# Performance work log

Hardware: AMD Instinct MI355X
Metric: run time of the kernel (lower is better)

Reference implementation:

```python
import jax, jax.numpy as jnp
import numpy as np

B, F, D = 1024, 64, 64  # batch, num fields, embedding dim


def setup_inputs() -> dict:
    key = jax.random.key(0)
    ks = jax.random.split(key, 7)
    return {
        "x": jax.random.normal(ks[0], (B, F, D), dtype=jnp.float32),
        "W1": jax.random.normal(ks[1], (F, F * F), dtype=jnp.float32) * 0.02,
        "b1": jax.random.normal(ks[2], (F,), dtype=jnp.float32) * 0.02,
        "W2": jax.random.normal(ks[3], (F, F * F), dtype=jnp.float32) * 0.02,
        "b2": jax.random.normal(ks[4], (F,), dtype=jnp.float32) * 0.02,
        "Wfc": jax.random.normal(ks[5], (1, 2 * F), dtype=jnp.float32) * 0.02,
        "bfc": jax.random.normal(ks[6], (1,), dtype=jnp.float32) * 0.02,
    }


def reference(x, W1, b1, W2, b2, Wfc, bfc):
    # x: [B, F, D]. CIN layer: outer product over field dims, 1x1 conv (channel
    # contraction with weight [F, F*F]), ReLU.
    b_, f0, d = x.shape
    x0 = x[:, :, None, :]  # [B, F, 1, D]
    h = x
    xs = []
    for W, b in ((W1, b1), (W2, b2)):
        z = (x0 * h[:, None, :, :]).reshape(b_, f0 * f0, d)  # [B, F*F, D]
        h = jax.nn.relu(jnp.einsum('oc,bcd->bod', W, z) + b[None, :, None])  # [B, F, D]
        xs.append(h)
    pooled = jnp.sum(jnp.concatenate(xs, axis=1), axis=2)  # [B, 2F] sum-pool over D
    return pooled @ Wfc.T + bfc  # [B, 1]
```

## Files before the change

### kernel.cpp

```cpp
#include <hip/hip_runtime.h>

typedef short s16x4 __attribute__((ext_vector_type(4)));
typedef short s16x8 __attribute__((ext_vector_type(8)));
typedef float f32x2 __attribute__((ext_vector_type(2)));
typedef float f32x16 __attribute__((ext_vector_type(16)));
typedef unsigned int u32x4 __attribute__((ext_vector_type(4)));

#define HT_STRIDE 72

__device__ __forceinline__ unsigned short f2bf(float f) {
    unsigned int u = __float_as_uint(f);
    u += 0x7fffu + ((u >> 16) & 1u);
    return (unsigned short)(u >> 16);
}
__device__ __forceinline__ float bf2f(unsigned short h) {
    return __uint_as_float(((unsigned int)h) << 16);
}
__device__ __forceinline__ unsigned int pk2bf_rne(float lo, float hi) {
    unsigned int a = __float_as_uint(lo);
    a += 0x7fffu + ((a >> 16) & 1u);
    unsigned int b = __float_as_uint(hi);
    b += 0x7fffu + ((b >> 16) & 1u);
    return (a >> 16) | (b & 0xffff0000u);
}

__global__ __launch_bounds__(256) void prepack_kernel(const float* __restrict__ W1,
                                                      const float* __restrict__ W2,
                                                      unsigned short* __restrict__ Wp) {
    int tid = blockIdx.x * 256 + threadIdx.x;
    int lane = tid & 63;
    int ks = (tid >> 6) & 3;
    int jt = (tid >> 8) & 1;
    int o = (tid >> 9) & 63;
    int l = tid >> 15;
    int q2 = lane >> 5;
    int n31 = lane & 31;
    const float* W = l ? W2 : W1;
    const float* base = W + o * 4096 + jt * 32 + n31;
    int i0 = 16 * ks + 8 * q2;
    float v[8];
#pragma unroll
    for (int t = 0; t < 8; ++t) v[t] = base[(i0 + t) * 64];
    u32x4 pv;
    pv[0] = pk2bf_rne(v[0], v[1]);
    pv[1] = pk2bf_rne(v[2], v[3]);
    pv[2] = pk2bf_rne(v[4], v[5]);
    pv[3] = pk2bf_rne(v[6], v[7]);
    ((u32x4*)Wp)[tid] = pv;
}

__global__ __launch_bounds__(256, 2) void cin_kernel(const float* __restrict__ x,
                                                     const unsigned short* __restrict__ Wp,
                                                     const float* __restrict__ b1,
                                                     const float* __restrict__ b2,
                                                     const float* __restrict__ Wfc,
                                                     const float* __restrict__ bfc,
                                                     float* __restrict__ out) {
    __shared__ __align__(16) unsigned short sH[2][2][64 * HT_STRIDE];
    __shared__ float sBias[128], sWfc[128], sRed[4];

    const int tid = threadIdx.x;
    const int w = tid >> 6;
    const int lane = tid & 63;
    const int q2 = lane >> 5;
    const int n31 = lane & 31;
    const int b_loc = w & 1;
    const int oh = w >> 1;
    const int bb = blockIdx.x;

#pragma unroll
    for (int bl = 0; bl < 2; ++bl) {
        const float4* xb4 = (const float4*)(x + (bb * 2 + bl) * 4096);
#pragma unroll
        for (int rr = 0; rr < 4; ++rr) {
            int e4 = rr * 256 + tid;
            float4 v = xb4[e4];
            int e = e4 << 2;
            int f = e >> 6;
            int d0 = e & 63;
            sH[0][bl][(d0 + 0) * HT_STRIDE + f] = f2bf(v.x);
            sH[0][bl][(d0 + 1) * HT_STRIDE + f] = f2bf(v.y);
            sH[0][bl][(d0 + 2) * HT_STRIDE + f] = f2bf(v.z);
            sH[0][bl][(d0 + 3) * HT_STRIDE + f] = f2bf(v.w);
        }
    }
    if (tid < 128) {
        sBias[tid] = (tid < 64) ? b1[tid] : b2[tid - 64];
        sWfc[tid] = Wfc[tid];
    }
    __syncthreads();

    const f32x16 zz = {};
    float contrib = 0.0f;
    const s16x8* WpS8 = (const s16x8*)Wp;

    s16x8 bfr[2][4];
#pragma unroll
    for (int nt = 0; nt < 2; ++nt) {
        const int d = nt * 32 + n31;
#pragma unroll
        for (int ks = 0; ks < 4; ++ks)
            bfr[nt][ks] = *(const s16x8*)&sH[0][b_loc][d * HT_STRIDE + 16 * ks + 8 * q2];
    }

    for (int l = 0; l < 2; ++l) {
        if (l) __syncthreads();

        const unsigned short* hsrc = sH[l][b_loc];
        f32x2 cw[2][2][8];
#pragma unroll
        for (int nt = 0; nt < 2; ++nt) {
            const int d = nt * 32 + n31;
#pragma unroll
            for (int jt = 0; jt < 2; ++jt)
#pragma unroll
                for (int m = 0; m < 4; ++m) {
                    s16x4 hv = *(const s16x4*)&hsrc[d * HT_STRIDE + jt * 32 + 4 * q2 + 8 * m];
                    cw[nt][jt][2 * m] = (f32x2){bf2f((unsigned short)hv[0]),
                                                bf2f((unsigned short)hv[1])};
                    cw[nt][jt][2 * m + 1] = (f32x2){bf2f((unsigned short)hv[2]),
                                                    bf2f((unsigned short)hv[3])};
                }
        }

        s16x8 Areg[2][4];
        {
            const int F0 = (l * 128 + 2 * oh) * 4;
            const s16x8* p = WpS8 + F0 * 64 + lane;
#pragma unroll
            for (int ks = 0; ks < 4; ++ks) Areg[0][ks] = p[ks * 64];
        }
        f32x2 hp[2];

#pragma unroll 2
        for (int it = 0; it < 64; ++it) {
            const int oc = it >> 1, jt = it & 1;
            const int o = 2 * oc + oh;
            if (it < 63) {
                const int itn = it + 1;
                const int on = 2 * (itn >> 1) + oh;
                const int Fn = (l * 128 + 2 * on + (itn & 1)) * 4;
                const s16x8* p = WpS8 + Fn * 64 + lane;
#pragma unroll
                for (int ks = 0; ks < 4; ++ks) Areg[(it + 1) & 1][ks] = p[ks * 64];
            }
            const s16x8* A = Areg[it & 1];

            f32x16 a0 = __builtin_amdgcn_mfma_f32_32x32x16_bf16(A[0], bfr[0][0], zz, 0, 0, 0);
            f32x16 a1 = __builtin_amdgcn_mfma_f32_32x32x16_bf16(A[0], bfr[1][0], zz, 0, 0, 0);
#pragma unroll
            for (int ks = 1; ks < 4; ++ks) {
                a0 = __builtin_amdgcn_mfma_f32_32x32x16_bf16(A[ks], bfr[0][ks], a0, 0, 0, 0);
                a1 = __builtin_amdgcn_mfma_f32_32x32x16_bf16(A[ks], bfr[1][ks], a1, 0, 0, 0);
            }

#pragma unroll
            for (int nt = 0; nt < 2; ++nt) {
                const f32x2* a2 = nt ? (const f32x2*)&a1 : (const f32x2*)&a0;
                f32x2 s = a2[0] * cw[nt][jt][0];
#pragma unroll
                for (int p = 1; p < 8; ++p) s += a2[p] * cw[nt][jt][p];
                if (jt == 0) {
                    hp[nt] = s;
                } else {
                    f32x2 t2 = hp[nt] + s;
                    float hsum = t2.x + t2.y;
                    hsum += __shfl_xor(hsum, 32, 64);
                    float v = fmaxf(hsum + sBias[l * 64 + o], 0.0f);
                    contrib += v * sWfc[l * 64 + o];
                    if (l == 0)
                        sH[1][b_loc][(nt * 32 + n31) * HT_STRIDE + o] = f2bf(v);
                }
            }
        }
    }

    contrib *= 0.5f;
#pragma unroll
    for (int off = 32; off > 0; off >>= 1)
        contrib += __shfl_down(contrib, off, 64);
    if (lane == 0) sRed[w] = contrib;
    __syncthreads();
    if (tid < 2)
        out[bb * 2 + tid] = sRed[tid] + sRed[tid + 2] + bfc[0];
}

extern "C" void kernel_launch(void* const* d_in, const int* in_sizes, int n_in,
                              void* d_out, int out_size, void* d_ws, size_t ws_size,
                              hipStream_t stream) {
    const float* x = (const float*)d_in[0];
    const float* W1 = (const float*)d_in[1];
    const float* b1 = (const float*)d_in[2];
    const float* W2 = (const float*)d_in[3];
    const float* b2 = (const float*)d_in[4];
    const float* Wfc = (const float*)d_in[5];
    const float* bfc = (const float*)d_in[6];
    float* out = (float*)d_out;

    unsigned short* Wp = (unsigned short*)d_ws;

    prepack_kernel<<<256, 256, 0, stream>>>(W1, W2, Wp);
    cin_kernel<<<512, 256, 0, stream>>>(x, Wp, b1, b2, Wfc, bfc, out);
}
```

Baseline: 137.8 us.

## Split CIN work one batch per block with four waves over output channels

Each block now handles a single batch element, with its four waves splitting the 64 output channels into groups of four instead of two batches times two channel halves. The grid doubles to 1024 blocks, LDS per block halves, and launch bounds allow four blocks per CU, so more work is in flight and each wave runs half as many MFMA iterations. The prepack kernel now stages a full weight row in LDS for coalesced reads and writes the bf16 fragments in a layout ordered by wave group, so each wave streams its weights contiguously. The trade-off is that each weight fragment is now loaded once per batch element rather than being shared across two batches in a block, which doubles weight traffic through L2.

```diff
diff --git a/kernel.cpp b/kernel.cpp
--- a/kernel.cpp
+++ b/kernel.cpp
@@ -27,50 +27,55 @@
 __global__ __launch_bounds__(256) void prepack_kernel(const float* __restrict__ W1,
                                                       const float* __restrict__ W2,
                                                       unsigned short* __restrict__ Wp) {
-    int tid = blockIdx.x * 256 + threadIdx.x;
-    int lane = tid & 63;
-    int ks = (tid >> 6) & 3;
-    int jt = (tid >> 8) & 1;
-    int o = (tid >> 9) & 63;
-    int l = tid >> 15;
-    int q2 = lane >> 5;
-    int n31 = lane & 31;
+    __shared__ float sRow[4096];
+    const int blk = blockIdx.x;
+    const int l = blk >> 6, o = blk & 63;
     const float* W = l ? W2 : W1;
-    const float* base = W + o * 4096 + jt * 32 + n31;
-    int i0 = 16 * ks + 8 * q2;
-    float v[8];
-#pragma unroll
-    for (int t = 0; t < 8; ++t) v[t] = base[(i0 + t) * 64];
-    u32x4 pv;
-    pv[0] = pk2bf_rne(v[0], v[1]);
-    pv[1] = pk2bf_rne(v[2], v[3]);
-    pv[2] = pk2bf_rne(v[4], v[5]);
-    pv[3] = pk2bf_rne(v[6], v[7]);
-    ((u32x4*)Wp)[tid] = pv;
-}
-
-__global__ __launch_bounds__(256, 2) void cin_kernel(const float* __restrict__ x,
+    const float4* src = (const float4*)(W + o * 4096);
+    float4* dstL = (float4*)sRow;
+#pragma unroll
+    for (int r = 0; r < 4; ++r)
+        dstL[r * 256 + threadIdx.x] = src[r * 256 + threadIdx.x];
+    __syncthreads();
+    const int oh = o & 3, oc = o >> 2;
+#pragma unroll
+    for (int s = 0; s < 2; ++s) {
+        int sl = s * 256 + threadIdx.x;
+        int lane = sl & 63;
+        int ks = (sl >> 6) & 3;
+        int jt = sl >> 8;
+        int q2 = lane >> 5, n31 = lane & 31;
+        const float* base = sRow + jt * 32 + n31;
+        int i0 = 16 * ks + 8 * q2;
+        u32x4 pv;
+        pv[0] = pk2bf_rne(base[(i0 + 0) * 64], base[(i0 + 1) * 64]);
+        pv[1] = pk2bf_rne(base[(i0 + 2) * 64], base[(i0 + 3) * 64]);
+        pv[2] = pk2bf_rne(base[(i0 + 4) * 64], base[(i0 + 5) * 64]);
+        pv[3] = pk2bf_rne(base[(i0 + 6) * 64], base[(i0 + 7) * 64]);
+        int G = (((l * 4 + oh) * 16 + oc) * 2 + jt) * 4 + ks;
+        ((u32x4*)Wp)[G * 64 + lane] = pv;
+    }
+}
+
+__global__ __launch_bounds__(256, 4) void cin_kernel(const float* __restrict__ x,
                                                      const unsigned short* __restrict__ Wp,
                                                      const float* __restrict__ b1,
                                                      const float* __restrict__ b2,
                                                      const float* __restrict__ Wfc,
                                                      const float* __restrict__ bfc,
                                                      float* __restrict__ out) {
-    __shared__ __align__(16) unsigned short sH[2][2][64 * HT_STRIDE];
+    __shared__ __align__(16) unsigned short sH[2][64 * HT_STRIDE];
     __shared__ float sBias[128], sWfc[128], sRed[4];
 
     const int tid = threadIdx.x;
-    const int w = tid >> 6;
+    const int oh = tid >> 6;
     const int lane = tid & 63;
     const int q2 = lane >> 5;
     const int n31 = lane & 31;
-    const int b_loc = w & 1;
-    const int oh = w >> 1;
     const int bb = blockIdx.x;
 
-#pragma unroll
-    for (int bl = 0; bl < 2; ++bl) {
-        const float4* xb4 = (const float4*)(x + (bb * 2 + bl) * 4096);
+    {
+        const float4* xb4 = (const float4*)(x + bb * 4096);
 #pragma unroll
         for (int rr = 0; rr < 4; ++rr) {
             int e4 = rr * 256 + tid;
@@ -78,10 +83,10 @@
             int e = e4 << 2;
             int f = e >> 6;
             int d0 = e & 63;
-            sH[0][bl][(d0 + 0) * HT_STRIDE + f] = f2bf(v.x);
-            sH[0][bl][(d0 + 1) * HT_STRIDE + f] = f2bf(v.y);
-            sH[0][bl][(d0 + 2) * HT_STRIDE + f] = f2bf(v.z);
-            sH[0][bl][(d0 + 3) * HT_STRIDE + f] = f2bf(v.w);
+            sH[0][(d0 + 0) * HT_STRIDE + f] = f2bf(v.x);
+            sH[0][(d0 + 1) * HT_STRIDE + f] = f2bf(v.y);
+            sH[0][(d0 + 2) * HT_STRIDE + f] = f2bf(v.z);
+            sH[0][(d0 + 3) * HT_STRIDE + f] = f2bf(v.w);
         }
     }
     if (tid < 128) {
@@ -100,13 +105,13 @@
         const int d = nt * 32 + n31;
 #pragma unroll
         for (int ks = 0; ks < 4; ++ks)
-            bfr[nt][ks] = *(const s16x8*)&sH[0][b_loc][d * HT_STRIDE + 16 * ks + 8 * q2];
+            bfr[nt][ks] = *(const s16x8*)&sH[0][d * HT_STRIDE + 16 * ks + 8 * q2];
     }
 
     for (int l = 0; l < 2; ++l) {
         if (l) __syncthreads();
 
-        const unsigned short* hsrc = sH[l][b_loc];
+        const unsigned short* hsrc = sH[l];
         f32x2 cw[2][2][8];
 #pragma unroll
         for (int nt = 0; nt < 2; ++nt) {
@@ -123,24 +128,18 @@
                 }
         }
 
+        const s16x8* pW = WpS8 + (l * 4 + oh) * 128 * 64 + lane;
         s16x8 Areg[2][4];
-        {
-            const int F0 = (l * 128 + 2 * oh) * 4;
-            const s16x8* p = WpS8 + F0 * 64 + lane;
-#pragma unroll
-            for (int ks = 0; ks < 4; ++ks) Areg[0][ks] = p[ks * 64];
-        }
+#pragma unroll
+        for (int ks = 0; ks < 4; ++ks) Areg[0][ks] = pW[ks * 64];
         f32x2 hp[2];
 
 #pragma unroll 2
-        for (int it = 0; it < 64; ++it) {
-            const int oc = it >> 1, jt = it & 1;
-            const int o = 2 * oc + oh;
-            if (it < 63) {
-                const int itn = it + 1;
-                const int on = 2 * (itn >> 1) + oh;
-                const int Fn = (l * 128 + 2 * on + (itn & 1)) * 4;
-                const s16x8* p = WpS8 + Fn * 64 + lane;
+        for (int it = 0; it < 32; ++it) {
+            const int jt = it & 1;
+            const int o = 4 * (it >> 1) + oh;
+            if (it < 31) {
+                const s16x8* p = pW + (it + 1) * 4 * 64;
 #pragma unroll
                 for (int ks = 0; ks < 4; ++ks) Areg[(it + 1) & 1][ks] = p[ks * 64];
             }
@@ -169,7 +168,7 @@
                     float v = fmaxf(hsum + sBias[l * 64 + o], 0.0f);
                     contrib += v * sWfc[l * 64 + o];
                     if (l == 0)
-                        sH[1][b_loc][(nt * 32 + n31) * HT_STRIDE + o] = f2bf(v);
+                        sH[1][(nt * 32 + n31) * HT_STRIDE + o] = f2bf(v);
                 }
             }
         }
@@ -179,10 +178,10 @@
 #pragma unroll
     for (int off = 32; off > 0; off >>= 1)
         contrib += __shfl_down(contrib, off, 64);
-    if (lane == 0) sRed[w] = contrib;
+    if (lane == 0) sRed[oh] = contrib;
     __syncthreads();
-    if (tid < 2)
-        out[bb * 2 + tid] = sRed[tid] + sRed[tid + 2] + bfc[0];
+    if (tid == 0)
+        out[bb] = sRed[0] + sRed[1] + sRed[2] + sRed[3] + bfc[0];
 }
 
 extern "C" void kernel_launch(void* const* d_in, const int* in_sizes, int n_in,
@@ -199,6 +198,6 @@
 
     unsigned short* Wp = (unsigned short*)d_ws;
 
-    prepack_kernel<<<256, 256, 0, stream>>>(W1, W2, Wp);
-    cin_kernel<<<512, 256, 0, stream>>>(x, Wp, b1, b2, Wfc, bfc, out);
-}
+    prepack_kernel<<<128, 256, 0, stream>>>(W1, W2, Wp);
+    cin_kernel<<<1024, 256, 0, stream>>>(x, Wp, b1, b2, Wfc, bfc, out);
+}
```

After: 338.9 us. 146% more time.
